# Kernel optimization log

Measured on AMD Instinct MI355X. Metric: run time of the kernel, lower is better.

## Reference

```python
import jax, jax.numpy as jnp
from jax import lax
import numpy as np

B, T, L = 32, 2048, 100
HID = 512   # LSTM hidden = hidden_dim*2 (hidden_dim=256)
E = 64      # embedding_dim (== target_size, required so step-0 input width matches)
V = 64      # target_size


def setup_inputs() -> dict:
    key = jax.random.key(0)
    ks = jax.random.split(key, 16)
    s = 0.05
    ins = [E + HID, HID, HID]
    d = {
        "context_tensor": jax.random.normal(ks[0], (B, T, HID), jnp.float32),
        "ground_truth": jax.random.randint(ks[1], (B, L), 0, V, dtype=jnp.int32),
        "tf_rate": 1,
        "embedding": jax.random.normal(ks[2], (V, E), jnp.float32) * s,
        "w_out": jax.random.normal(ks[3], (V, 2 * HID), jnp.float32) * s,
        "b_out": jnp.zeros((V,), jnp.float32),
    }
    for l in range(3):
        d[f"w_ih{l}"] = jax.random.normal(ks[4 + 4 * l], (4 * HID, ins[l]), jnp.float32) * s
        d[f"w_hh{l}"] = jax.random.normal(ks[5 + 4 * l], (4 * HID, HID), jnp.float32) * s
        d[f"b_ih{l}"] = jax.random.normal(ks[6 + 4 * l], (4 * HID,), jnp.float32) * s
        d[f"b_hh{l}"] = jax.random.normal(ks[7 + 4 * l], (4 * HID,), jnp.float32) * s
    return d


def _forward(context_tensor, ground_truth, embedding, lstm_params, w_out, b_out):
    dt = context_tensor.dtype
    gt_emb = embedding[ground_truth]                                  # [B, L, E]
    seed = jax.nn.one_hot(ground_truth[:, 0], V, dtype=dt)            # [B, V]
    rnn_in0 = jnp.concatenate([seed, context_tensor[:, 0, :]], -1)    # [B, E+HID]
    h0 = jnp.zeros((3, HID), dt)
    c0 = jnp.zeros((3, HID), dt)

    def lstm_cell(carry, x):
        # 3-layer LSTMCell step; torch gate order i, f, g, o
        h, c = carry
        hs, cs = [], []
        inp = x
        for l, (w_ih, w_hh, b_ih, b_hh) in enumerate(lstm_params):
            g = w_ih @ inp + b_ih + w_hh @ h[l] + b_hh
            i, f, gg, o = jnp.split(g, 4)
            c_new = jax.nn.sigmoid(f) * c[l] + jax.nn.sigmoid(i) * jnp.tanh(gg)
            h_new = jax.nn.sigmoid(o) * jnp.tanh(c_new)
            hs.append(h_new)
            cs.append(c_new)
            inp = h_new
        return (jnp.stack(hs), jnp.stack(cs)), inp

    def step(carry, gt_next):
        rnn_in, h, c = carry
        # Faithful to torch: LSTM has batch_first=False, so the [B,1,feat] input
        # is scanned along the BATCH axis with batch=1; state carries across steps.
        (h, c), rnn_out = lax.scan(lstm_cell, (h, c), rnn_in)        # [B, HID]
        energy = jnp.einsum('bd,btd->bt', rnn_out, context_tensor)   # [B, T]
        att = jax.nn.softmax(energy, axis=-1)
        ctx = jnp.einsum('bt,btd->bd', att, context_tensor)           # [B, HID]
        feat = jnp.concatenate([rnn_out, ctx], axis=-1)               # [B, 2*HID]
        pred = jax.nn.log_softmax(feat @ w_out.T + b_out, axis=-1)    # [B, V]
        new_in = jnp.concatenate([gt_next, ctx], axis=-1)             # teacher forcing
        return (new_in, h, c), pred

    xs = jnp.swapaxes(gt_emb[:, 1:, :], 0, 1)                         # [L-1, B, E]
    _, preds = lax.scan(step, (rnn_in0, h0, c0), xs)                  # [L-1, B, V]
    return jnp.swapaxes(preds, 0, 1)                                  # [B, L-1, V]


def reference(context_tensor, ground_truth, tf_rate, embedding,
              w_ih0, w_hh0, b_ih0, b_hh0,
              w_ih1, w_hh1, b_ih1, b_hh1,
              w_ih2, w_hh2, b_ih2, b_hh2,
              w_out, b_out):
    del tf_rate  # fixed to 1 -> always teacher forcing (deterministic)
    params = [(w_ih0, w_hh0, b_ih0, b_hh0),
              (w_ih1, w_hh1, b_ih1, b_hh1),
              (w_ih2, w_hh2, b_ih2, b_hh2)]
    return _forward(context_tensor, ground_truth, embedding, params, w_out, b_out)
```

## Files before the change

kernel.cpp:

```cpp
#include <hip/hip_runtime.h>
#include <math.h>

#define NBLK 128
#define NTHR 512
#define NPOS 3168
#define NSTAGES 3177
#define HIDN 512
#define TT 2048
#define LL 100

__device__ __forceinline__ float aload(const float* p) {
  return __hip_atomic_load((float*)p, __ATOMIC_RELAXED, __HIP_MEMORY_SCOPE_AGENT);
}
__device__ __forceinline__ void astore(float* p, float v) {
  __hip_atomic_store(p, v, __ATOMIC_RELAXED, __HIP_MEMORY_SCOPE_AGENT);
}
__device__ __forceinline__ int aload_i(const int* p) {
  return __hip_atomic_load((int*)p, __ATOMIC_RELAXED, __HIP_MEMORY_SCOPE_AGENT);
}
__device__ __forceinline__ void astore_i(int* p, int v) {
  __hip_atomic_store(p, v, __ATOMIC_RELAXED, __HIP_MEMORY_SCOPE_AGENT);
}
__device__ __forceinline__ float wsum(float v) {
#pragma unroll
  for (int o = 32; o; o >>= 1) v += __shfl_xor(v, o);
  return v;
}
__device__ __forceinline__ float wmax(float v) {
#pragma unroll
  for (int o = 32; o; o >>= 1) v = fmaxf(v, __shfl_xor(v, o));
  return v;
}
__device__ __forceinline__ float sigm(float x) { return 1.f / (1.f + expf(-x)); }

extern "C" __global__ void speller_init(float* ws) {
  const int i = blockIdx.x * blockDim.x + threadIdx.x;
  if (i < 5120) ws[i] = 0.f;
}

extern "C" __global__ __launch_bounds__(NTHR, 2)
void speller_main(const float* __restrict__ ctx_t, const int* __restrict__ gt,
                  const float* __restrict__ emb, const float* __restrict__ w_out,
                  const float* __restrict__ b_out,
                  const float* __restrict__ wi0, const float* __restrict__ wh0,
                  const float* __restrict__ bi0, const float* __restrict__ bh0,
                  const float* __restrict__ wi1, const float* __restrict__ wh1,
                  const float* __restrict__ bi1, const float* __restrict__ bh1,
                  const float* __restrict__ wi2, const float* __restrict__ wh2,
                  const float* __restrict__ bi2, const float* __restrict__ bh2,
                  float* __restrict__ out, float* __restrict__ ws)
{
  const int bid = blockIdx.x, tid = threadIdx.x;
  const int lane = tid & 63, wv = tid >> 6;
  const int ub = bid * 4;

  int*   arrive   = (int*)ws;
  float* h_buf    = ws + 2048;
  float* rnn_ring = ws + 5120;
  float* ctx_ring = ws + 9216;
  float* e_ring   = ws + 41984;
  float* w_ring   = ws + 46080;
  float* P_ring   = ws + 50176;
  float* Q_ring   = ws + 181248;
  float* z_ring   = ws + 197632;

  __shared__ float sro[HIDN];
  __shared__ float swex[16];
  __shared__ float gates[48];
  __shared__ float csto[12];

  if (tid < 12) csto[tid] = 0.f;

  const int lyr = wv >> 1;
  float wreg[8][17];
  float bsum[8];
  if (wv < 6) {
    if (lyr == 0) {
#pragma unroll
      for (int r = 0; r < 8; ++r) {
        const int R = (wv * 2 + (r >> 2)) * 512 + ub + (r & 3);
#pragma unroll
        for (int k = 0; k < 9; ++k) wreg[r][k] = wi0[(size_t)R * 576 + k * 64 + lane];
#pragma unroll
        for (int k = 0; k < 8; ++k) wreg[r][9 + k] = wh0[(size_t)R * 512 + k * 64 + lane];
        bsum[r] = bi0[R] + bh0[R];
      }
    } else {
      const float* wiL = (lyr == 1) ? wi1 : wi2;
      const float* whL = (lyr == 1) ? wh1 : wh2;
      const float* biL = (lyr == 1) ? bi1 : bi2;
      const float* bhL = (lyr == 1) ? bh1 : bh2;
#pragma unroll
      for (int r = 0; r < 8; ++r) {
        const int R = ((wv & 1) * 2 + (r >> 2)) * 512 + ub + (r & 3);
#pragma unroll
        for (int k = 0; k < 8; ++k) wreg[r][k] = wiL[(size_t)R * 512 + k * 64 + lane];
#pragma unroll
        for (int k = 0; k < 8; ++k) wreg[r][8 + k] = whL[(size_t)R * 512 + k * 64 + lane];
        bsum[r] = biL[R] + bhL[R];
      }
    }
  }
  float wp[16];
  float bz = 0.f;
  if (bid < 64 && wv == 6) {
#pragma unroll
    for (int k = 0; k < 16; ++k) wp[k] = w_out[(size_t)bid * 1024 + k * 64 + lane];
    bz = b_out[bid];
  }

  for (int s = 0; s < NSTAGES; ++s) {
    const float* hb = h_buf + (s & 1) * 1536;
    const int p1 = s - 3, p2 = s - 4, p3 = s - 5, p4 = s - 6,
              p5 = s - 7, p6 = s - 8, p7 = s - 9;

    if (p1 >= 0 && p1 < NPOS) sro[tid] = aload(rnn_ring + (p1 & 7) * 512 + tid);
    if (p3 >= 0 && p3 < NPOS && tid < 16)
      swex[tid] = aload(w_ring + (p3 & 1) * 2048 + bid * 16 + tid);

    if (wv < 6) {
      const int pL = s - lyr;
      if (pL >= 0 && pL < NPOS) {
        float x[17];
        if (lyr == 0) {
          const int b0 = s & 31, t0 = s >> 5;
          const int g0 = gt[b0 * LL + t0];
          if (t0 == 0) {
            x[0] = (lane == g0) ? 1.f : 0.f;
            const float* cb = ctx_t + (size_t)b0 * TT * HIDN;
#pragma unroll
            for (int k = 0; k < 8; ++k) x[1 + k] = cb[k * 64 + lane];
          } else {
            x[0] = emb[g0 * 64 + lane];
            const float* cr = ctx_ring + ((s - 32) & 63) * 512;
#pragma unroll
            for (int k = 0; k < 8; ++k) x[1 + k] = aload(cr + k * 64 + lane);
          }
#pragma unroll
          for (int k = 0; k < 8; ++k) x[9 + k] = aload(hb + k * 64 + lane);
#pragma unroll
          for (int r = 0; r < 8; ++r) {
            float a = 0.f;
#pragma unroll
            for (int k = 0; k < 17; ++k) a += wreg[r][k] * x[k];
            a = wsum(a) + bsum[r];
            if (lane == 0) gates[(wv * 2 + (r >> 2)) * 4 + (r & 3)] = a;
          }
        } else {
          const int base = (lyr - 1) * 512;
          float xx[16];
#pragma unroll
          for (int k = 0; k < 8; ++k) xx[k]     = aload(hb + base + k * 64 + lane);
#pragma unroll
          for (int k = 0; k < 8; ++k) xx[8 + k] = aload(hb + base + 512 + k * 64 + lane);
#pragma unroll
          for (int r = 0; r < 8; ++r) {
            float a = 0.f;
#pragma unroll
            for (int k = 0; k < 16; ++k) a += wreg[r][k] * xx[k];
            a = wsum(a) + bsum[r];
            if (lane == 0) gates[lyr * 16 + ((wv & 1) * 2 + (r >> 2)) * 4 + (r & 3)] = a;
          }
        }
      }
    }
    __syncthreads();

    if (tid < 12) {
      const int l = tid >> 2, q = tid & 3;
      const int pl = s - l;
      if (pl >= 0 && pl < NPOS) {
        const float gi = gates[l * 16 + q];
        const float gf = gates[l * 16 + 4 + q];
        const float gg = gates[l * 16 + 8 + q];
        const float go = gates[l * 16 + 12 + q];
        const float cn = sigm(gf) * csto[tid] + sigm(gi) * tanhf(gg);
        const float hn = sigm(go) * tanhf(cn);
        csto[tid] = cn;
        const int u = ub + q;
        astore(h_buf + ((s + 1) & 1) * 1536 + l * 512 + u, hn);
        if (l == 2) astore(rnn_ring + (pl & 7) * 512 + u, hn);
      }
    }

    if (p1 >= 0 && p1 < NPOS) {
      const int b1 = p1 & 31;
#pragma unroll
      for (int jj = 0; jj < 2; ++jj) {
        const int j = bid * 16 + wv * 2 + jj;
        const float* crow = ctx_t + ((size_t)b1 * TT + j) * HIDN;
        float a = 0.f;
#pragma unroll
        for (int k = 0; k < 8; ++k) a += crow[k * 64 + lane] * sro[k * 64 + lane];
        a = wsum(a);
        if (lane == 0) astore(e_ring + (p1 & 1) * 2048 + j, a);
      }
    }

    if (p3 >= 0 && p3 < NPOS) {
      const int b3 = p3 & 31;
      const float* cb3 = ctx_t + ((size_t)b3 * TT + bid * 16) * HIDN;
      float* Pb = P_ring + (p3 & 1) * (128 * 512) + bid * 512;
      for (int c = tid; c < 512; c += NTHR) {
        float a0 = 0.f;
#pragma unroll
        for (int j = 0; j < 16; ++j) a0 += swex[j] * cb3[j * HIDN + c];
        astore(Pb + c, a0);
      }
    }

    if (bid < 16 && p4 >= 0 && p4 < NPOS) {
      const float* Pb = P_ring + (p4 & 1) * (128 * 512) + (bid * 8) * 512;
      float* Qb = Q_ring + (p4 & 1) * 8192 + bid * 512;
      for (int c = tid; c < 512; c += NTHR) {
        float q0 = 0.f;
#pragma unroll
        for (int k = 0; k < 8; ++k) q0 += aload(Pb + k * 512 + c);
        astore(Qb + c, q0);
      }
    }

    if (bid == 16 && p5 >= 0 && p5 < NPOS) {
      const float* Qb = Q_ring + (p5 & 1) * 8192;
      float* cr = ctx_ring + (p5 & 63) * 512;
      for (int c = tid; c < 512; c += NTHR) {
        float c0 = 0.f;
#pragma unroll
        for (int k = 0; k < 16; ++k) c0 += aload(Qb + k * 512 + c);
        astore(cr + c, c0);
      }
    }

    if (bid == 17 && wv == 7 && p2 >= 0 && p2 < NPOS) {
      const float* eb = e_ring + (p2 & 1) * 2048;
      float e[32];
#pragma unroll
      for (int k = 0; k < 32; ++k) e[k] = aload(eb + k * 64 + lane);
      float m = e[0];
#pragma unroll
      for (int k = 1; k < 32; ++k) m = fmaxf(m, e[k]);
      m = wmax(m);
      float ssum = 0.f;
#pragma unroll
      for (int k = 0; k < 32; ++k) { e[k] = expf(e[k] - m); ssum += e[k]; }
      ssum = wsum(ssum);
      const float inv = 1.f / ssum;
      float* wb = w_ring + (p2 & 1) * 2048;
#pragma unroll
      for (int k = 0; k < 32; ++k) astore(wb + k * 64 + lane, e[k] * inv);
    }

    if (bid < 64 && wv == 6 && p6 >= 0 && p6 < NPOS) {
      const float* rr6 = rnn_ring + (p6 & 7) * 512;
      const float* cr6 = ctx_ring + (p6 & 63) * 512;
      float a = 0.f;
#pragma unroll
      for (int k = 0; k < 8; ++k) a += wp[k] * aload(rr6 + k * 64 + lane);
#pragma unroll
      for (int k = 0; k < 8; ++k) a += wp[8 + k] * aload(cr6 + k * 64 + lane);
      a = wsum(a);
      if (lane == 0) astore(z_ring + (p6 & 1) * 64 + bid, a + bz);
    }

    if (bid == 18 && wv == 7 && p7 >= 0 && p7 < NPOS) {
      const float z = aload(z_ring + (p7 & 1) * 64 + lane);
      const float M = wmax(z);
      const float ls = M + logf(wsum(expf(z - M)));
      out[((size_t)(p7 & 31) * 99 + (p7 >> 5)) * 64 + lane] = z - ls;
    }

    asm volatile("s_waitcnt vmcnt(0)" ::: "memory");
    __syncthreads();
    if (tid == 0) astore_i(arrive + bid * 16, s + 1);
    if (tid < NBLK)
      while (aload_i(arrive + tid * 16) < s + 1) __builtin_amdgcn_s_sleep(1);
    asm volatile("" ::: "memory");
    __syncthreads();
  }
}

extern "C" void kernel_launch(void* const* d_in, const int* in_sizes, int n_in,
                              void* d_out, int out_size, void* d_ws, size_t ws_size,
                              hipStream_t stream) {
  (void)in_sizes; (void)n_in; (void)out_size; (void)ws_size;
  const float* ctx_t = (const float*)d_in[0];
  const int*   gt    = (const int*)d_in[1];
  const float* emb   = (const float*)d_in[3];
  const float* w_out = (const float*)d_in[4];
  const float* b_out = (const float*)d_in[5];
  const float* wi0 = (const float*)d_in[6];
  const float* wh0 = (const float*)d_in[7];
  const float* bi0 = (const float*)d_in[8];
  const float* bh0 = (const float*)d_in[9];
  const float* wi1 = (const float*)d_in[10];
  const float* wh1 = (const float*)d_in[11];
  const float* bi1 = (const float*)d_in[12];
  const float* bh1 = (const float*)d_in[13];
  const float* wi2 = (const float*)d_in[14];
  const float* wh2 = (const float*)d_in[15];
  const float* bi2 = (const float*)d_in[16];
  const float* bh2 = (const float*)d_in[17];
  float* out = (float*)d_out;
  float* ws  = (float*)d_ws;

  hipLaunchKernelGGL(speller_init, dim3(20), dim3(256), 0, stream, ws);

  hipLaunchKernelGGL(speller_main, dim3(NBLK), dim3(NTHR), 0, stream,
                     ctx_t, gt, emb, w_out, b_out,
                     wi0, wh0, bi0, bh0,
                     wi1, wh1, bi1, bh1,
                     wi2, wh2, bi2, bh2,
                     out, ws);
}
```

Measured before the change: 24.47 ms.

## Split per-stage grid barrier into two flags and prefetch context rows

Replaces the single end-of-stage grid barrier with two flag sets. The h flag is published right after the LSTM cell update, and the full-stage flag is waited on only before the attention-weight consumers, so recurrent work can overlap with the tail of the previous stage. The context rows for the weighted-sum stage and the rnn_out values are loaded into registers early to hide latency, the e_ring depth grows to 4, and the reduction roles move to blocks 64-82 so they do not collide with the LSTM blocks. This adds a second spin-wait per stage and extra register pressure, and the cross-stage hazard reasoning becomes subtler.

```diff
diff --git a/kernel.cpp b/kernel.cpp
--- a/kernel.cpp
+++ b/kernel.cpp
@@ -35,7 +35,7 @@
 
 extern "C" __global__ void speller_init(float* ws) {
   const int i = blockIdx.x * blockDim.x + threadIdx.x;
-  if (i < 5120) ws[i] = 0.f;
+  if (i < 7168) ws[i] = 0.f;
 }
 
 extern "C" __global__ __launch_bounds__(NTHR, 2)
@@ -54,15 +54,16 @@
   const int lane = tid & 63, wv = tid >> 6;
   const int ub = bid * 4;
 
-  int*   arrive   = (int*)ws;
-  float* h_buf    = ws + 2048;
-  float* rnn_ring = ws + 5120;
-  float* ctx_ring = ws + 9216;
-  float* e_ring   = ws + 41984;
-  float* w_ring   = ws + 46080;
-  float* P_ring   = ws + 50176;
-  float* Q_ring   = ws + 181248;
-  float* z_ring   = ws + 197632;
+  int*   hflag    = (int*)ws;
+  int*   fflag    = (int*)ws + 2048;
+  float* h_buf    = ws + 4096;
+  float* rnn_ring = ws + 7168;
+  float* ctx_ring = ws + 11264;
+  float* e_ring   = ws + 44032;
+  float* w_ring   = ws + 52224;
+  float* P_ring   = ws + 56320;
+  float* Q_ring   = ws + 187392;
+  float* z_ring   = ws + 203776;
 
   __shared__ float sro[HIDN];
   __shared__ float swex[16];
@@ -114,15 +115,31 @@
     const int p1 = s - 3, p2 = s - 4, p3 = s - 5, p4 = s - 6,
               p5 = s - 7, p6 = s - 8, p7 = s - 9;
 
+    if (tid < NBLK)
+      while (aload_i(hflag + tid * 16) < s) __builtin_amdgcn_s_sleep(1);
+    asm volatile("" ::: "memory");
+    __syncthreads();
+
     if (p1 >= 0 && p1 < NPOS) sro[tid] = aload(rnn_ring + (p1 & 7) * 512 + tid);
-    if (p3 >= 0 && p3 < NPOS && tid < 16)
-      swex[tid] = aload(w_ring + (p3 & 1) * 2048 + bid * 16 + tid);
+
+    float cc[16];
+    if (p3 >= 0 && p3 < NPOS) {
+      const float* cb3 = ctx_t + ((size_t)(p3 & 31) * TT + bid * 16) * HIDN;
+#pragma unroll
+      for (int j = 0; j < 16; ++j) cc[j] = cb3[j * HIDN + tid];
+    }
+    float r6[8];
+    if (bid < 64 && wv == 6 && p6 >= 0 && p6 < NPOS) {
+      const float* rr6 = rnn_ring + (p6 & 7) * 512;
+#pragma unroll
+      for (int k = 0; k < 8; ++k) r6[k] = aload(rr6 + k * 64 + lane);
+    }
 
     if (wv < 6) {
       const int pL = s - lyr;
       if (pL >= 0 && pL < NPOS) {
-        float x[17];
         if (lyr == 0) {
+          float x[17];
           const int b0 = s & 31, t0 = s >> 5;
           const int g0 = gt[b0 * LL + t0];
           if (t0 == 0) {
@@ -182,6 +199,10 @@
         if (l == 2) astore(rnn_ring + (pl & 7) * 512 + u, hn);
       }
     }
+    if (wv == 0) {
+      asm volatile("s_waitcnt vmcnt(0)" ::: "memory");
+      if (tid == 0) astore_i(hflag + bid * 16, s + 1);
+    }
 
     if (p1 >= 0 && p1 < NPOS) {
       const int b1 = p1 & 31;
@@ -193,46 +214,44 @@
 #pragma unroll
         for (int k = 0; k < 8; ++k) a += crow[k * 64 + lane] * sro[k * 64 + lane];
         a = wsum(a);
-        if (lane == 0) astore(e_ring + (p1 & 1) * 2048 + j, a);
-      }
-    }
+        if (lane == 0) astore(e_ring + (p1 & 3) * 2048 + j, a);
+      }
+    }
+
+    if (tid < NBLK)
+      while (aload_i(fflag + tid * 16) < s) __builtin_amdgcn_s_sleep(1);
+    asm volatile("" ::: "memory");
+    __syncthreads();
+    if (p3 >= 0 && p3 < NPOS && tid < 16)
+      swex[tid] = aload(w_ring + (p3 & 1) * 2048 + bid * 16 + tid);
+    __syncthreads();
 
     if (p3 >= 0 && p3 < NPOS) {
-      const int b3 = p3 & 31;
-      const float* cb3 = ctx_t + ((size_t)b3 * TT + bid * 16) * HIDN;
-      float* Pb = P_ring + (p3 & 1) * (128 * 512) + bid * 512;
-      for (int c = tid; c < 512; c += NTHR) {
-        float a0 = 0.f;
-#pragma unroll
-        for (int j = 0; j < 16; ++j) a0 += swex[j] * cb3[j * HIDN + c];
-        astore(Pb + c, a0);
-      }
-    }
-
-    if (bid < 16 && p4 >= 0 && p4 < NPOS) {
-      const float* Pb = P_ring + (p4 & 1) * (128 * 512) + (bid * 8) * 512;
-      float* Qb = Q_ring + (p4 & 1) * 8192 + bid * 512;
-      for (int c = tid; c < 512; c += NTHR) {
-        float q0 = 0.f;
-#pragma unroll
-        for (int k = 0; k < 8; ++k) q0 += aload(Pb + k * 512 + c);
-        astore(Qb + c, q0);
-      }
-    }
-
-    if (bid == 16 && p5 >= 0 && p5 < NPOS) {
+      float a = 0.f;
+#pragma unroll
+      for (int j = 0; j < 16; ++j) a += swex[j] * cc[j];
+      astore(P_ring + (p3 & 1) * (128 * 512) + bid * 512 + tid, a);
+    }
+
+    if (bid >= 64 && bid < 80 && p4 >= 0 && p4 < NPOS) {
+      const int i = bid - 64;
+      const float* Pb = P_ring + (p4 & 1) * (128 * 512);
+      float q0 = 0.f;
+#pragma unroll
+      for (int k = 0; k < 8; ++k) q0 += aload(Pb + (i * 8 + k) * 512 + tid);
+      astore(Q_ring + (p4 & 1) * 8192 + i * 512 + tid, q0);
+    }
+
+    if (bid == 80 && p5 >= 0 && p5 < NPOS) {
       const float* Qb = Q_ring + (p5 & 1) * 8192;
-      float* cr = ctx_ring + (p5 & 63) * 512;
-      for (int c = tid; c < 512; c += NTHR) {
-        float c0 = 0.f;
-#pragma unroll
-        for (int k = 0; k < 16; ++k) c0 += aload(Qb + k * 512 + c);
-        astore(cr + c, c0);
-      }
-    }
-
-    if (bid == 17 && wv == 7 && p2 >= 0 && p2 < NPOS) {
-      const float* eb = e_ring + (p2 & 1) * 2048;
+      float c0 = 0.f;
+#pragma unroll
+      for (int k = 0; k < 16; ++k) c0 += aload(Qb + k * 512 + tid);
+      astore(ctx_ring + (p5 & 63) * 512 + tid, c0);
+    }
+
+    if (bid == 81 && wv == 7 && p2 >= 0 && p2 < NPOS) {
+      const float* eb = e_ring + (p2 & 3) * 2048;
       float e[32];
 #pragma unroll
       for (int k = 0; k < 32; ++k) e[k] = aload(eb + k * 64 + lane);
@@ -251,18 +270,17 @@
     }
 
     if (bid < 64 && wv == 6 && p6 >= 0 && p6 < NPOS) {
-      const float* rr6 = rnn_ring + (p6 & 7) * 512;
       const float* cr6 = ctx_ring + (p6 & 63) * 512;
       float a = 0.f;
 #pragma unroll
-      for (int k = 0; k < 8; ++k) a += wp[k] * aload(rr6 + k * 64 + lane);
-#pragma unroll
       for (int k = 0; k < 8; ++k) a += wp[8 + k] * aload(cr6 + k * 64 + lane);
+#pragma unroll
+      for (int k = 0; k < 8; ++k) a += wp[k] * r6[k];
       a = wsum(a);
       if (lane == 0) astore(z_ring + (p6 & 1) * 64 + bid, a + bz);
     }
 
-    if (bid == 18 && wv == 7 && p7 >= 0 && p7 < NPOS) {
+    if (bid == 82 && wv == 7 && p7 >= 0 && p7 < NPOS) {
       const float z = aload(z_ring + (p7 & 1) * 64 + lane);
       const float M = wmax(z);
       const float ls = M + logf(wsum(expf(z - M)));
@@ -271,11 +289,7 @@
 
     asm volatile("s_waitcnt vmcnt(0)" ::: "memory");
     __syncthreads();
-    if (tid == 0) astore_i(arrive + bid * 16, s + 1);
-    if (tid < NBLK)
-      while (aload_i(arrive + tid * 16) < s + 1) __builtin_amdgcn_s_sleep(1);
-    asm volatile("" ::: "memory");
-    __syncthreads();
+    if (tid == 0) astore_i(fflag + bid * 16, s + 1);
   }
 }
 
@@ -303,7 +317,7 @@
   float* out = (float*)d_out;
   float* ws  = (float*)d_ws;
 
-  hipLaunchKernelGGL(speller_init, dim3(20), dim3(256), 0, stream, ws);
+  hipLaunchKernelGGL(speller_init, dim3(28), dim3(256), 0, stream, ws);
 
   hipLaunchKernelGGL(speller_main, dim3(NBLK), dim3(NTHR), 0, stream,
                      ctx_t, gt, emb, w_out, b_out,
```

New measurement: 44.93 ms. 1.84x slower.

## Prefetch context rows during barrier wait and hoist ring loads ahead of LSTM compute

Applied to the files above, without the earlier changes.

Input-independent context rows for the attention energy and the weighted-sum stages are now loaded into registers between posting this block's arrival flag and spinning on the grid barrier, so their latency overlaps the barrier wait. Ring-buffer reads for the reduction, softmax, output projection and log-softmax stages are issued at the start of each stage, ahead of the LSTM gate compute. The small single-block reduction tasks move to otherwise idle block ids (64–82) so they no longer share blocks with LSTM work. The e_ring grows to four slots and the workspace offsets shift to match. The cost is higher register pressure from the new per-thread buffers, which may lower occupancy or cause spills.

```diff
diff --git a/kernel.cpp b/kernel.cpp
--- a/kernel.cpp
+++ b/kernel.cpp
@@ -59,10 +59,10 @@
   float* rnn_ring = ws + 5120;
   float* ctx_ring = ws + 9216;
   float* e_ring   = ws + 41984;
-  float* w_ring   = ws + 46080;
-  float* P_ring   = ws + 50176;
-  float* Q_ring   = ws + 181248;
-  float* z_ring   = ws + 197632;
+  float* w_ring   = ws + 50176;
+  float* P_ring   = ws + 54272;
+  float* Q_ring   = ws + 185344;
+  float* z_ring   = ws + 201728;
 
   __shared__ float sro[HIDN];
   __shared__ float swex[16];
@@ -109,6 +109,8 @@
     bz = b_out[bid];
   }
 
+  float ca0[8], ca1[8], cc[16];
+
   for (int s = 0; s < NSTAGES; ++s) {
     const float* hb = h_buf + (s & 1) * 1536;
     const int p1 = s - 3, p2 = s - 4, p3 = s - 5, p4 = s - 6,
@@ -118,11 +120,43 @@
     if (p3 >= 0 && p3 < NPOS && tid < 16)
       swex[tid] = aload(w_ring + (p3 & 1) * 2048 + bid * 16 + tid);
 
+    float pp[8];
+    if (bid >= 64 && bid < 80 && p4 >= 0 && p4 < NPOS) {
+      const float* Pb = P_ring + (p4 & 1) * (128 * 512) + ((bid - 64) * 8) * 512;
+#pragma unroll
+      for (int k = 0; k < 8; ++k) pp[k] = aload(Pb + k * 512 + tid);
+    }
+    float qq[16];
+    if (bid == 80 && p5 >= 0 && p5 < NPOS) {
+      const float* Qb = Q_ring + (p5 & 1) * 8192;
+#pragma unroll
+      for (int k = 0; k < 16; ++k) qq[k] = aload(Qb + k * 512 + tid);
+    }
+    float ee[32];
+    if (bid == 81 && wv == 7 && p2 >= 0 && p2 < NPOS) {
+      const float* eb = e_ring + (p2 & 3) * 2048;
+#pragma unroll
+      for (int k = 0; k < 32; ++k) ee[k] = aload(eb + k * 64 + lane);
+    }
+    float r6[8], c6[8];
+    if (bid < 64 && wv == 6 && p6 >= 0 && p6 < NPOS) {
+      const float* rr6 = rnn_ring + (p6 & 7) * 512;
+      const float* cr6 = ctx_ring + (p6 & 63) * 512;
+#pragma unroll
+      for (int k = 0; k < 8; ++k) {
+        r6[k] = aload(rr6 + k * 64 + lane);
+        c6[k] = aload(cr6 + k * 64 + lane);
+      }
+    }
+    float zz = 0.f;
+    if (bid == 82 && wv == 7 && p7 >= 0 && p7 < NPOS)
+      zz = aload(z_ring + (p7 & 1) * 64 + lane);
+
     if (wv < 6) {
       const int pL = s - lyr;
       if (pL >= 0 && pL < NPOS) {
-        float x[17];
         if (lyr == 0) {
+          float x[17];
           const int b0 = s & 31, t0 = s >> 5;
           const int g0 = gt[b0 * LL + t0];
           if (t0 == 0) {
@@ -184,94 +218,93 @@
     }
 
     if (p1 >= 0 && p1 < NPOS) {
-      const int b1 = p1 & 31;
-#pragma unroll
-      for (int jj = 0; jj < 2; ++jj) {
-        const int j = bid * 16 + wv * 2 + jj;
-        const float* crow = ctx_t + ((size_t)b1 * TT + j) * HIDN;
-        float a = 0.f;
-#pragma unroll
-        for (int k = 0; k < 8; ++k) a += crow[k * 64 + lane] * sro[k * 64 + lane];
-        a = wsum(a);
-        if (lane == 0) astore(e_ring + (p1 & 1) * 2048 + j, a);
+      float a0 = 0.f, a1 = 0.f;
+#pragma unroll
+      for (int k = 0; k < 8; ++k) {
+        a0 += ca0[k] * sro[k * 64 + lane];
+        a1 += ca1[k] * sro[k * 64 + lane];
+      }
+      a0 = wsum(a0);
+      a1 = wsum(a1);
+      if (lane == 0) {
+        float* eb = e_ring + (p1 & 3) * 2048 + bid * 16 + wv * 2;
+        astore(eb, a0);
+        astore(eb + 1, a1);
       }
     }
 
     if (p3 >= 0 && p3 < NPOS) {
-      const int b3 = p3 & 31;
-      const float* cb3 = ctx_t + ((size_t)b3 * TT + bid * 16) * HIDN;
-      float* Pb = P_ring + (p3 & 1) * (128 * 512) + bid * 512;
-      for (int c = tid; c < 512; c += NTHR) {
-        float a0 = 0.f;
-#pragma unroll
-        for (int j = 0; j < 16; ++j) a0 += swex[j] * cb3[j * HIDN + c];
-        astore(Pb + c, a0);
-      }
-    }
-
-    if (bid < 16 && p4 >= 0 && p4 < NPOS) {
-      const float* Pb = P_ring + (p4 & 1) * (128 * 512) + (bid * 8) * 512;
-      float* Qb = Q_ring + (p4 & 1) * 8192 + bid * 512;
-      for (int c = tid; c < 512; c += NTHR) {
-        float q0 = 0.f;
-#pragma unroll
-        for (int k = 0; k < 8; ++k) q0 += aload(Pb + k * 512 + c);
-        astore(Qb + c, q0);
-      }
-    }
-
-    if (bid == 16 && p5 >= 0 && p5 < NPOS) {
-      const float* Qb = Q_ring + (p5 & 1) * 8192;
-      float* cr = ctx_ring + (p5 & 63) * 512;
-      for (int c = tid; c < 512; c += NTHR) {
-        float c0 = 0.f;
-#pragma unroll
-        for (int k = 0; k < 16; ++k) c0 += aload(Qb + k * 512 + c);
-        astore(cr + c, c0);
-      }
-    }
-
-    if (bid == 17 && wv == 7 && p2 >= 0 && p2 < NPOS) {
-      const float* eb = e_ring + (p2 & 1) * 2048;
-      float e[32];
-#pragma unroll
-      for (int k = 0; k < 32; ++k) e[k] = aload(eb + k * 64 + lane);
-      float m = e[0];
-#pragma unroll
-      for (int k = 1; k < 32; ++k) m = fmaxf(m, e[k]);
+      float a = 0.f;
+#pragma unroll
+      for (int j = 0; j < 16; ++j) a += swex[j] * cc[j];
+      astore(P_ring + (p3 & 1) * (128 * 512) + bid * 512 + tid, a);
+    }
+
+    if (bid >= 64 && bid < 80 && p4 >= 0 && p4 < NPOS) {
+      float q0 = 0.f;
+#pragma unroll
+      for (int k = 0; k < 8; ++k) q0 += pp[k];
+      astore(Q_ring + (p4 & 1) * 8192 + (bid - 64) * 512 + tid, q0);
+    }
+
+    if (bid == 80 && p5 >= 0 && p5 < NPOS) {
+      float c0 = 0.f;
+#pragma unroll
+      for (int k = 0; k < 16; ++k) c0 += qq[k];
+      astore(ctx_ring + (p5 & 63) * 512 + tid, c0);
+    }
+
+    if (bid == 81 && wv == 7 && p2 >= 0 && p2 < NPOS) {
+      float m = ee[0];
+#pragma unroll
+      for (int k = 1; k < 32; ++k) m = fmaxf(m, ee[k]);
       m = wmax(m);
       float ssum = 0.f;
 #pragma unroll
-      for (int k = 0; k < 32; ++k) { e[k] = expf(e[k] - m); ssum += e[k]; }
+      for (int k = 0; k < 32; ++k) { ee[k] = expf(ee[k] - m); ssum += ee[k]; }
       ssum = wsum(ssum);
       const float inv = 1.f / ssum;
       float* wb = w_ring + (p2 & 1) * 2048;
 #pragma unroll
-      for (int k = 0; k < 32; ++k) astore(wb + k * 64 + lane, e[k] * inv);
+      for (int k = 0; k < 32; ++k) astore(wb + k * 64 + lane, ee[k] * inv);
     }
 
     if (bid < 64 && wv == 6 && p6 >= 0 && p6 < NPOS) {
-      const float* rr6 = rnn_ring + (p6 & 7) * 512;
-      const float* cr6 = ctx_ring + (p6 & 63) * 512;
       float a = 0.f;
 #pragma unroll
-      for (int k = 0; k < 8; ++k) a += wp[k] * aload(rr6 + k * 64 + lane);
-#pragma unroll
-      for (int k = 0; k < 8; ++k) a += wp[8 + k] * aload(cr6 + k * 64 + lane);
+      for (int k = 0; k < 8; ++k) a += wp[k] * r6[k] + wp[8 + k] * c6[k];
       a = wsum(a);
       if (lane == 0) astore(z_ring + (p6 & 1) * 64 + bid, a + bz);
     }
 
-    if (bid == 18 && wv == 7 && p7 >= 0 && p7 < NPOS) {
-      const float z = aload(z_ring + (p7 & 1) * 64 + lane);
-      const float M = wmax(z);
-      const float ls = M + logf(wsum(expf(z - M)));
-      out[((size_t)(p7 & 31) * 99 + (p7 >> 5)) * 64 + lane] = z - ls;
+    if (bid == 82 && wv == 7 && p7 >= 0 && p7 < NPOS) {
+      const float M = wmax(zz);
+      const float ls = M + logf(wsum(expf(zz - M)));
+      out[((size_t)(p7 & 31) * 99 + (p7 >> 5)) * 64 + lane] = zz - ls;
     }
 
     asm volatile("s_waitcnt vmcnt(0)" ::: "memory");
     __syncthreads();
     if (tid == 0) astore_i(arrive + bid * 16, s + 1);
+
+    {
+      const int p1n = s - 2;
+      if (p1n >= 0 && p1n < NPOS) {
+        const float* c0p = ctx_t + ((size_t)(p1n & 31) * TT + bid * 16 + wv * 2) * HIDN;
+#pragma unroll
+        for (int k = 0; k < 8; ++k) {
+          ca0[k] = c0p[k * 64 + lane];
+          ca1[k] = c0p[HIDN + k * 64 + lane];
+        }
+      }
+      const int p3n = s - 4;
+      if (p3n >= 0 && p3n < NPOS) {
+        const float* cb3 = ctx_t + ((size_t)(p3n & 31) * TT + bid * 16) * HIDN;
+#pragma unroll
+        for (int j = 0; j < 16; ++j) cc[j] = cb3[j * HIDN + tid];
+      }
+    }
+
     if (tid < NBLK)
       while (aload_i(arrive + tid * 16) < s + 1) __builtin_amdgcn_s_sleep(1);
     asm volatile("" ::: "memory");
```

Measured after the change: 48.14 ms. 96.7% more time.
